# Performance work log

Hardware: AMD Instinct MI355X
Metric: run time of the kernel (lower is better)

Reference implementation:

```python
import jax, jax.numpy as jnp
import numpy as np

N, IN, C, H, NC, E, G = 4096, 16, 128, 2, 4, 131072, 64
EPS = 1e-5


def setup_inputs() -> dict:
    key = jax.random.key(0)
    ks = jax.random.split(key, 12)
    def rn(k, shape, scale=0.05):
        return jax.random.normal(k, shape, dtype=jnp.float32) * scale
    return dict(
        x=rn(ks[0], (N, IN), 1.0),
        edge_index=jax.random.randint(ks[1], (2, E), 0, N, dtype=jnp.int32),
        batch=jnp.sort(jax.random.randint(ks[2], (N,), 0, G, dtype=jnp.int32)),
        proj_W=rn(ks[3], (IN, C)), proj_b=jnp.zeros((C,), jnp.float32),
        gcn_W=rn(ks[4], (2, C, C)), gcn_b=jnp.zeros((2, C), jnp.float32),
        attn_qkv_w=rn(ks[5], (2, 3 * C, C)), attn_qkv_b=jnp.zeros((2, 3 * C), jnp.float32),
        attn_out_w=rn(ks[6], (2, C, C)), attn_out_b=jnp.zeros((2, C), jnp.float32),
        bn_gamma=jnp.ones((2, 3, C), jnp.float32), bn_beta=jnp.zeros((2, 3, C), jnp.float32),
        mlp_W1=rn(ks[7], (2, C, 2 * C)), mlp_b1=jnp.zeros((2, 2 * C), jnp.float32),
        mlp_W2=rn(ks[8], (2, 2 * C, C)), mlp_b2=jnp.zeros((2, C), jnp.float32),
        lin_W=rn(ks[9], (C, NC)), lin_b=jnp.zeros((NC,), jnp.float32),
    )


def _bn(h, g, b):
    # PyG BatchNorm (training-mode stats over the node dim, biased var)
    mu = jnp.mean(h, axis=0)
    var = jnp.mean((h - mu) ** 2, axis=0)
    return (h - mu) * jax.lax.rsqrt(var + EPS) * g + b


def _gcn(h_in, W, b, src, dst):
    # GCNConv: x' = D^-1/2 (A+I) D^-1/2 (x W) + b
    h = h_in @ W
    deg = jnp.zeros((N,), h.dtype).at[dst].add(1.0) + 1.0  # +1 self loop
    dinv = jax.lax.rsqrt(deg)
    coef = dinv[src] * dinv[dst]                           # [E]
    out = jax.ops.segment_sum(h[src] * coef[:, None], dst, num_segments=N)
    out = out + h * (dinv * dinv)[:, None]                 # self-loop term
    return out + b


def _mha(x, wqkv, bqkv, wout, bout):
    # batch=None in the source => attention over all N nodes as one sequence
    qkv = x @ wqkv.T + bqkv                                # [N,3C]
    q, k, v = jnp.split(qkv, 3, axis=-1)
    dh = C // H
    q = q.reshape(N, H, dh) * (dh ** -0.5)
    k = k.reshape(N, H, dh)
    v = v.reshape(N, H, dh)
    a = jax.nn.softmax(jnp.einsum('nhd,mhd->hnm', q, k), axis=-1)  # [H,N,N]
    o = jnp.einsum('hnm,mhd->nhd', a, v).reshape(N, C)
    return o @ wout.T + bout


def _forward(x, proj_W, proj_b, gcn_W, gcn_b, attn_qkv_w, attn_qkv_b,
             attn_out_w, attn_out_b, bn_gamma, bn_beta, mlp_W1, mlp_b1,
             mlp_W2, mlp_b2, lin_W, lin_b, edge_index, batch):
    src, dst = edge_index[0], edge_index[1]
    h = x @ proj_W + proj_b
    for l in range(2):  # two structurally-distinct GPS layers
        hl = _bn(_gcn(h, gcn_W[l], gcn_b[l], src, dst) + h, bn_gamma[l, 0], bn_beta[l, 0])
        ha = _bn(_mha(h, attn_qkv_w[l], attn_qkv_b[l], attn_out_w[l], attn_out_b[l]) + h,
                 bn_gamma[l, 1], bn_beta[l, 1])
        o = hl + ha
        m = jax.nn.relu(o @ mlp_W1[l] + mlp_b1[l]) @ mlp_W2[l] + mlp_b2[l]
        h = _bn(o + m, bn_gamma[l, 2], bn_beta[l, 2])
        if l == 0:
            h = jax.nn.relu(h)
    ssum = jax.ops.segment_sum(h, batch, num_segments=G)
    cnt = jax.ops.segment_sum(jnp.ones((N,), h.dtype), batch, num_segments=G)
    pooled = ssum / jnp.maximum(cnt, 1.0)[:, None]
    return pooled @ lin_W + lin_b


def reference(x, edge_index, batch, proj_W, proj_b, gcn_W, gcn_b,
              attn_qkv_w, attn_qkv_b, attn_out_w, attn_out_b,
              bn_gamma, bn_beta, mlp_W1, mlp_b1, mlp_W2, mlp_b2,
              lin_W, lin_b):
    return _forward(x, proj_W, proj_b, gcn_W, gcn_b, attn_qkv_w, attn_qkv_b,
                    attn_out_w, attn_out_b, bn_gamma, bn_beta, mlp_W1, mlp_b1,
                    mlp_W2, mlp_b2, lin_W, lin_b, edge_index, batch)
```

## Files before the change

kernel.cpp:

```cpp
#include <hip/hip_runtime.h>
#include <hip/hip_bf16.h>


constexpr int N_  = 4096;
constexpr int IN_ = 16;
constexpr int C_  = 128;
constexpr int E_  = 131072;
constexpr int G_  = 64;
constexpr float EPSV = 1e-5f;
constexpr int SP_ = 8;

typedef unsigned short u16;
typedef __attribute__((ext_vector_type(8))) short bf16x8;
typedef __attribute__((ext_vector_type(8))) unsigned short u16x8;
typedef __attribute__((ext_vector_type(4))) float f32x4;

__device__ inline u16 f2bf(float f) {
  union { __hip_bfloat16 b; u16 u; } v;
  v.b = __float2bfloat16(f);
  return v.u;
}
__device__ inline float bf2f(u16 s) {
  union { unsigned u; float f; } v; v.u = ((unsigned)s) << 16;
  return v.f;
}

__global__ __launch_bounds__(256) void proj_k(const float* __restrict__ x,
                                              const float* __restrict__ W,
                                              const float* __restrict__ b,
                                              float* __restrict__ h) {
  int idx = blockIdx.x * 256 + threadIdx.x;
  int n = idx >> 7, c = idx & 127;
  float acc = b[c];
#pragma unroll
  for (int k = 0; k < IN_; ++k) acc = fmaf(x[n * IN_ + k], W[k * C_ + c], acc);
  h[idx] = acc;
}

__global__ __launch_bounds__(256) void count_k(const int* __restrict__ ei,
                                               int* __restrict__ cnt) {
  int e = blockIdx.x * 256 + threadIdx.x;
  atomicAdd(&cnt[ei[E_ + e]], 1);
}
__global__ __launch_bounds__(256) void scan_k(const int* __restrict__ cnt,
                                              int* __restrict__ rowptr,
                                              int* __restrict__ cursor,
                                              float* __restrict__ dinv) {
  __shared__ int part[256];
  const int t = threadIdx.x;
  int v[16], s = 0;
#pragma unroll
  for (int i = 0; i < 16; ++i) { v[i] = cnt[t * 16 + i]; s += v[i]; }
  part[t] = s;
  __syncthreads();
  if (t == 0) {
    int run = 0;
    for (int i = 0; i < 256; ++i) { int x = part[i]; part[i] = run; run += x; }
  }
  __syncthreads();
  int off = part[t];
#pragma unroll
  for (int i = 0; i < 16; ++i) {
    int n = t * 16 + i;
    rowptr[n] = off; cursor[n] = off;
    dinv[n] = rsqrtf((float)v[i] + 1.0f);
    off += v[i];
  }
  if (t == 0) rowptr[N_] = E_;
}
__global__ __launch_bounds__(256) void fill_k(const int* __restrict__ ei,
                                              int* __restrict__ cursor,
                                              int* __restrict__ csr) {
  int e = blockIdx.x * 256 + threadIdx.x;
  int d = ei[E_ + e];
  int slot = atomicAdd(&cursor[d], 1);
  csr[slot] = ei[e];
}

__global__ __launch_bounds__(256) void wprep_k(const float* __restrict__ gcnW,
                                               const float* __restrict__ qkvW,
                                               const float* __restrict__ outW,
                                               const float* __restrict__ w1,
                                               const float* __restrict__ w2,
                                               u16* __restrict__ Wh,
                                               u16* __restrict__ Wl) {
  int bx = blockIdx.x;
  int l = bx / 144, b = bx % 144;
  const float* src; int dstOff, K, M, trans;
  if (b < 16)       { src = gcnW + l * 16384; dstOff = 0;      K = 128; M = 128; trans = 0; }
  else if (b < 64)  { src = qkvW + l * 49152; dstOff = 16384;  K = 128; M = 0;   trans = 1; b -= 16; }
  else if (b < 80)  { src = outW + l * 16384; dstOff = 65536;  K = 128; M = 0;   trans = 1; b -= 64; }
  else if (b < 112) { src = w1 + l * 32768;   dstOff = 81920;  K = 128; M = 256; trans = 0; b -= 80; }
  else              { src = w2 + l * 32768;   dstOff = 114688; K = 256; M = 128; trans = 0; b -= 112; }
  dstOff += l * 147456;
  int d = b * 1024 + threadIdx.x * 4;
  float v[4];
  if (trans) {
    const float4 f = *(const float4*)&src[d];
    v[0] = f.x; v[1] = f.y; v[2] = f.z; v[3] = f.w;
  } else {
    int ks = (K == 256) ? 8 : 7;
    int n = d >> ks, k = d & (K - 1);
#pragma unroll
    for (int j = 0; j < 4; ++j) v[j] = src[(size_t)(k + j) * M + n];
  }
  ushort4 hv, lv;
  u16* hp = (u16*)&hv; u16* lp = (u16*)&lv;
#pragma unroll
  for (int j = 0; j < 4; ++j) {
    u16 hh = f2bf(v[j]); hp[j] = hh; lp[j] = f2bf(v[j] - bf2f(hh));
  }
  *(ushort4*)&Wh[dstOff + d] = hv;
  *(ushort4*)&Wl[dstOff + d] = lv;
}

__global__ __launch_bounds__(256) void mgemm_dual_k(const float* __restrict__ A,
                                                    const u16* __restrict__ Bh,
                                                    const u16* __restrict__ Bl,
                                                    const float* __restrict__ qkvB,
                                                    float* __restrict__ t0,
                                                    u16* __restrict__ Qg,
                                                    u16* __restrict__ Kg,
                                                    u16* __restrict__ Vtg) {
  constexpr int LD = 72, K = 128;
  __shared__ u16 Ah[64 * LD], Al[64 * LD], Bsh[64 * LD], Bsl[64 * LD];
  const int tid = threadIdx.x;
  const int row0 = blockIdx.y * 64, col0 = blockIdx.x * 64;
  const int wv = tid >> 6, ln = tid & 63, quad = ln >> 4, c = ln & 15;
  f32x4 acc[4];
#pragma unroll
  for (int i = 0; i < 4; ++i) acc[i] = (f32x4){0.f, 0.f, 0.f, 0.f};

  for (int kt = 0; kt < K; kt += 64) {
    __syncthreads();
#pragma unroll
    for (int i = 0; i < 2; ++i) {
      int ch = tid + i * 256, r = ch >> 3, part = ch & 7;
      const float4 f0 = *(const float4*)&A[(size_t)(row0 + r) * K + kt + part * 8];
      const float4 f1 = *(const float4*)&A[(size_t)(row0 + r) * K + kt + part * 8 + 4];
      float fv[8] = {f0.x, f0.y, f0.z, f0.w, f1.x, f1.y, f1.z, f1.w};
      __attribute__((aligned(16))) u16 hb[8], lb[8];
#pragma unroll
      for (int j = 0; j < 8; ++j) {
        u16 hh = f2bf(fv[j]); hb[j] = hh; lb[j] = f2bf(fv[j] - bf2f(hh));
      }
      *(u16x8*)&Ah[r * LD + part * 8] = *(u16x8*)hb;
      *(u16x8*)&Al[r * LD + part * 8] = *(u16x8*)lb;
      size_t bo = (size_t)(col0 + r) * K + kt + part * 8;
      *(u16x8*)&Bsh[r * LD + part * 8] = *(const u16x8*)&Bh[bo];
      *(u16x8*)&Bsl[r * LD + part * 8] = *(const u16x8*)&Bl[bo];
    }
    __syncthreads();
#pragma unroll
    for (int kq = 0; kq < 2; ++kq) {
      bf16x8 ah = *(const bf16x8*)&Ah[(wv * 16 + c) * LD + kq * 32 + quad * 8];
      bf16x8 al = *(const bf16x8*)&Al[(wv * 16 + c) * LD + kq * 32 + quad * 8];
#pragma unroll
      for (int cb = 0; cb < 4; ++cb) {
        bf16x8 bh = *(const bf16x8*)&Bsh[(cb * 16 + c) * LD + kq * 32 + quad * 8];
        bf16x8 bl = *(const bf16x8*)&Bsl[(cb * 16 + c) * LD + kq * 32 + quad * 8];
        acc[cb] = __builtin_amdgcn_mfma_f32_16x16x32_bf16(al, bh, acc[cb], 0, 0, 0);
        acc[cb] = __builtin_amdgcn_mfma_f32_16x16x32_bf16(ah, bl, acc[cb], 0, 0, 0);
        acc[cb] = __builtin_amdgcn_mfma_f32_16x16x32_bf16(ah, bh, acc[cb], 0, 0, 0);
      }
    }
  }

  const int cls = blockIdx.x;
  if (cls < 2) {
#pragma unroll
    for (int cb = 0; cb < 4; ++cb)
#pragma unroll
      for (int r = 0; r < 4; ++r) {
        int rr = row0 + wv * 16 + quad * 4 + r;
        t0[(size_t)rr * 128 + col0 + cb * 16 + c] = acc[cb][r];
      }
  } else if (cls < 6) {
    const int isQ = cls < 4, h = cls & 1;
    const float sc = isQ ? 0.125f : 1.0f;
    u16* dst = isQ ? Qg : Kg;
#pragma unroll
    for (int cb = 0; cb < 4; ++cb) {
      int d = cb * 16 + c;
      float qb = qkvB[col0 - 128 + d];
#pragma unroll
      for (int r = 0; r < 4; ++r) {
        int rr = row0 + wv * 16 + quad * 4 + r;
        dst[((size_t)(h * N_ + rr)) * 64 + d] = f2bf((acc[cb][r] + qb) * sc);
      }
    }
  } else {
    const int h = cls & 1;
    u16* vtile = Ah;
    __syncthreads();
#pragma unroll
    for (int cb = 0; cb < 4; ++cb) {
      int d = cb * 16 + c;
      float vb = qkvB[col0 - 128 + d];
#pragma unroll
      for (int r = 0; r < 4; ++r)
        vtile[(wv * 16 + quad * 4 + r) * LD + d] = f2bf(acc[cb][r] + vb);
    }
    __syncthreads();
    int d = tid >> 2, j = tid & 3;
    __attribute__((aligned(16))) u16 buf[16];
#pragma unroll
    for (int m = 0; m < 16; ++m) buf[m] = vtile[(j * 16 + m) * LD + d];
    size_t o = ((size_t)(h * 64 + d)) * N_ + row0 + j * 16;
    *(u16x8*)&Vtg[o]     = *(u16x8*)&buf[0];
    *(u16x8*)&Vtg[o + 8] = *(u16x8*)&buf[8];
  }
}

__global__ __launch_bounds__(256) void mgemm_k(const float* __restrict__ A,
                                               const u16* __restrict__ Bh,
                                               const u16* __restrict__ Bl,
                                               const float* __restrict__ bias,
                                               float* __restrict__ Cout,
                                               int K, int Ncols, int relu,
                                               const float* __restrict__ resid,
                                               float* __restrict__ sums) {
  constexpr int LD = 72;
  __shared__ u16 Ah[64 * LD], Al[64 * LD], Bsh[64 * LD], Bsl[64 * LD];
  const int tid = threadIdx.x;
  const int row0 = blockIdx.y * 64, col0 = blockIdx.x * 64;
  const int wv = tid >> 6, ln = tid & 63, quad = ln >> 4, c = ln & 15;
  f32x4 acc[4];
#pragma unroll
  for (int i = 0; i < 4; ++i) acc[i] = (f32x4){0.f, 0.f, 0.f, 0.f};

  for (int kt = 0; kt < K; kt += 64) {
    __syncthreads();
#pragma unroll
    for (int i = 0; i < 2; ++i) {
      int ch = tid + i * 256, r = ch >> 3, part = ch & 7;
      const float4 f0 = *(const float4*)&A[(size_t)(row0 + r) * K + kt + part * 8];
      const float4 f1 = *(const float4*)&A[(size_t)(row0 + r) * K + kt + part * 8 + 4];
      float fv[8] = {f0.x, f0.y, f0.z, f0.w, f1.x, f1.y, f1.z, f1.w};
      __attribute__((aligned(16))) u16 hb[8], lb[8];
#pragma unroll
      for (int j = 0; j < 8; ++j) {
        u16 hh = f2bf(fv[j]); hb[j] = hh; lb[j] = f2bf(fv[j] - bf2f(hh));
      }
      *(u16x8*)&Ah[r * LD + part * 8] = *(u16x8*)hb;
      *(u16x8*)&Al[r * LD + part * 8] = *(u16x8*)lb;
      size_t bo = (size_t)(col0 + r) * K + kt + part * 8;
      *(u16x8*)&Bsh[r * LD + part * 8] = *(const u16x8*)&Bh[bo];
      *(u16x8*)&Bsl[r * LD + part * 8] = *(const u16x8*)&Bl[bo];
    }
    __syncthreads();
#pragma unroll
    for (int kq = 0; kq < 2; ++kq) {
      bf16x8 ah = *(const bf16x8*)&Ah[(wv * 16 + c) * LD + kq * 32 + quad * 8];
      bf16x8 al = *(const bf16x8*)&Al[(wv * 16 + c) * LD + kq * 32 + quad * 8];
#pragma unroll
      for (int cb = 0; cb < 4; ++cb) {
        bf16x8 bh = *(const bf16x8*)&Bsh[(cb * 16 + c) * LD + kq * 32 + quad * 8];
        bf16x8 bl = *(const bf16x8*)&Bsl[(cb * 16 + c) * LD + kq * 32 + quad * 8];
        acc[cb] = __builtin_amdgcn_mfma_f32_16x16x32_bf16(al, bh, acc[cb], 0, 0, 0);
        acc[cb] = __builtin_amdgcn_mfma_f32_16x16x32_bf16(ah, bl, acc[cb], 0, 0, 0);
        acc[cb] = __builtin_amdgcn_mfma_f32_16x16x32_bf16(ah, bh, acc[cb], 0, 0, 0);
      }
    }
  }
#pragma unroll
  for (int cb = 0; cb < 4; ++cb) {
    float s = 0.0f, s2 = 0.0f;
#pragma unroll
    for (int r = 0; r < 4; ++r) {
      int rr = row0 + wv * 16 + quad * 4 + r;
      int cc = col0 + cb * 16 + c;
      float o = acc[cb][r] + (bias ? bias[cc] : 0.0f);
      if (resid) o += resid[(size_t)rr * Ncols + cc];
      if (relu) o = fmaxf(o, 0.0f);
      Cout[(size_t)rr * Ncols + cc] = o;
      s += o; s2 = fmaf(o, o, s2);
    }
    if (sums) {
      s  += __shfl_xor(s, 16);  s  += __shfl_xor(s, 32);
      s2 += __shfl_xor(s2, 16); s2 += __shfl_xor(s2, 32);
      if (quad == 0) {
        int cc = col0 + cb * 16 + c;
        atomicAdd(&sums[cc], s);
        atomicAdd(&sums[C_ + cc], s2);
      }
    }
  }
}

__global__ __launch_bounds__(256) void mgemm_attn_k(const float* __restrict__ attnP,
                                                    const float* __restrict__ accLp,
                                                    const u16* __restrict__ Bh,
                                                    const u16* __restrict__ Bl,
                                                    const float* __restrict__ bias,
                                                    float* __restrict__ Cout,
                                                    const float* __restrict__ resid,
                                                    float* __restrict__ sums) {
  constexpr int LD = 72, K = 128;
  __shared__ u16 Ah[64 * LD], Al[64 * LD], Bsh[64 * LD], Bsl[64 * LD];
  const int tid = threadIdx.x;
  const int row0 = blockIdx.y * 64, col0 = blockIdx.x * 64;
  const int wv = tid >> 6, ln = tid & 63, quad = ln >> 4, c = ln & 15;
  f32x4 acc[4];
#pragma unroll
  for (int i = 0; i < 4; ++i) acc[i] = (f32x4){0.f, 0.f, 0.f, 0.f};

  for (int kt = 0; kt < K; kt += 64) {
    const int head = kt >> 6;
    __syncthreads();
#pragma unroll
    for (int i = 0; i < 2; ++i) {
      int ch = tid + i * 256, r = ch >> 3, part = ch & 7;
      float lsum = 0.0f;
#pragma unroll
      for (int sp = 0; sp < SP_; ++sp) lsum += accLp[(sp * 2 + head) * N_ + row0 + r];
      float invl = 1.0f / lsum;
      float fv[8] = {0.f, 0.f, 0.f, 0.f, 0.f, 0.f, 0.f, 0.f};
#pragma unroll
      for (int sp = 0; sp < SP_; ++sp) {
        const float* p = &attnP[((size_t)sp * N_ + row0 + r) * C_ + kt + part * 8];
        const float4 f0 = *(const float4*)p;
        const float4 f1 = *(const float4*)(p + 4);
        fv[0] += f0.x; fv[1] += f0.y; fv[2] += f0.z; fv[3] += f0.w;
        fv[4] += f1.x; fv[5] += f1.y; fv[6] += f1.z; fv[7] += f1.w;
      }
      __attribute__((aligned(16))) u16 hb[8], lb[8];
#pragma unroll
      for (int j = 0; j < 8; ++j) {
        float f = fv[j] * invl;
        u16 hh = f2bf(f); hb[j] = hh; lb[j] = f2bf(f - bf2f(hh));
      }
      *(u16x8*)&Ah[r * LD + part * 8] = *(u16x8*)hb;
      *(u16x8*)&Al[r * LD + part * 8] = *(u16x8*)lb;
      size_t bo = (size_t)(col0 + r) * K + kt + part * 8;
      *(u16x8*)&Bsh[r * LD + part * 8] = *(const u16x8*)&Bh[bo];
      *(u16x8*)&Bsl[r * LD + part * 8] = *(const u16x8*)&Bl[bo];
    }
    __syncthreads();
#pragma unroll
    for (int kq = 0; kq < 2; ++kq) {
      bf16x8 ah = *(const bf16x8*)&Ah[(wv * 16 + c) * LD + kq * 32 + quad * 8];
      bf16x8 al = *(const bf16x8*)&Al[(wv * 16 + c) * LD + kq * 32 + quad * 8];
#pragma unroll
      for (int cb = 0; cb < 4; ++cb) {
        bf16x8 bh = *(const bf16x8*)&Bsh[(cb * 16 + c) * LD + kq * 32 + quad * 8];
        bf16x8 bl = *(const bf16x8*)&Bsl[(cb * 16 + c) * LD + kq * 32 + quad * 8];
        acc[cb] = __builtin_amdgcn_mfma_f32_16x16x32_bf16(al, bh, acc[cb], 0, 0, 0);
        acc[cb] = __builtin_amdgcn_mfma_f32_16x16x32_bf16(ah, bl, acc[cb], 0, 0, 0);
        acc[cb] = __builtin_amdgcn_mfma_f32_16x16x32_bf16(ah, bh, acc[cb], 0, 0, 0);
      }
    }
  }
#pragma unroll
  for (int cb = 0; cb < 4; ++cb) {
    float s = 0.0f, s2 = 0.0f;
#pragma unroll
    for (int r = 0; r < 4; ++r) {
      int rr = row0 + wv * 16 + quad * 4 + r;
      int cc = col0 + cb * 16 + c;
      float o = acc[cb][r] + bias[cc] + resid[(size_t)rr * 128 + cc];
      Cout[(size_t)rr * 128 + cc] = o;
      s += o; s2 = fmaf(o, o, s2);
    }
    s  += __shfl_xor(s, 16);  s  += __shfl_xor(s, 32);
    s2 += __shfl_xor(s2, 16); s2 += __shfl_xor(s2, 32);
    if (quad == 0) {
      int cc = col0 + cb * 16 + c;
      atomicAdd(&sums[cc], s);
      atomicAdd(&sums[C_ + cc], s2);
    }
  }
}

__global__ __launch_bounds__(128) void gcn_gather_k(const int* __restrict__ rowptr,
                                                    const int* __restrict__ csr,
                                                    const float* __restrict__ hw,
                                                    const float* __restrict__ dinv,
                                                    const float* __restrict__ b,
                                                    const float* __restrict__ hres,
                                                    float* __restrict__ out) {
  const int n = blockIdx.x, c = threadIdx.x;
  const float din = dinv[n];
  float acc = fmaf(hw[(size_t)n * C_ + c], din * din, b[c] + hres[(size_t)n * C_ + c]);
  const int e1 = rowptr[n + 1];
  for (int e = rowptr[n]; e < e1; ++e) {
    int s = csr[e];
    acc = fmaf(hw[(size_t)s * C_ + c], dinv[s] * din, acc);
  }
  out[(size_t)n * C_ + c] = acc;
}

__global__ __launch_bounds__(256) void bn_stats_k(const float* __restrict__ A,
                                                  float* __restrict__ sums) {
  int c = threadIdx.x & 127, half = threadIdx.x >> 7;
  int r0 = blockIdx.x * 16 + half * 8;
  float s = 0.0f, s2 = 0.0f;
#pragma unroll
  for (int i = 0; i < 8; ++i) {
    float v = A[(size_t)(r0 + i) * C_ + c];
    s += v;
    s2 = fmaf(v, v, s2);
  }
  __shared__ float ls[256], ls2[256];
  ls[threadIdx.x] = s; ls2[threadIdx.x] = s2;
  __syncthreads();
  if (half == 0) {
    atomicAdd(&sums[c], s + ls[c + 128]);
    atomicAdd(&sums[C_ + c], s2 + ls2[c + 128]);
  }
}

__global__ __launch_bounds__(256) void bn_finapply2_k(const float* __restrict__ t0,
                                                      const float* __restrict__ t1,
                                                      const float* __restrict__ sums1,
                                                      const float* __restrict__ sums0,
                                                      const float* __restrict__ g1,
                                                      const float* __restrict__ b1v,
                                                      const float* __restrict__ g0,
                                                      const float* __restrict__ b0v,
                                                      float* __restrict__ ob) {
  __shared__ float scl1[128], shf1[128], scl0[128], shf0[128];
  const int t = threadIdx.x;
  if (t < 128) {
    float mu = sums1[t] * (1.0f / N_);
    float var = sums1[C_ + t] * (1.0f / N_) - mu * mu;
    float sc = rsqrtf(var + EPSV) * g1[t];
    scl1[t] = sc; shf1[t] = fmaf(-mu, sc, b1v[t]);
    mu = sums0[t] * (1.0f / N_);
    var = sums0[C_ + t] * (1.0f / N_) - mu * mu;
    sc = rsqrtf(var + EPSV) * g0[t];
    scl0[t] = sc; shf0[t] = fmaf(-mu, sc, b0v[t]);
  }
  __syncthreads();
  int idx = blockIdx.x * 256 + t;
  int c = idx & 127;
  ob[idx] = fmaf(t0[idx], scl1[c], shf1[c]) + fmaf(t1[idx], scl0[c], shf0[c]);
}

__global__ __launch_bounds__(256) void bn_finapply_k(const float* __restrict__ A,
                                                     const float* __restrict__ sums,
                                                     const float* __restrict__ g,
                                                     const float* __restrict__ b,
                                                     float* __restrict__ outp, int relu,
                                                     const int* __restrict__ batch,
                                                     float* __restrict__ pooled) {
  __shared__ float s_scl[128], s_shf[128];
  const int t = threadIdx.x;
  if (t < 128) {
    float mu = sums[t] * (1.0f / N_);
    float var = sums[C_ + t] * (1.0f / N_) - mu * mu;
    float sc = rsqrtf(var + EPSV) * g[t];
    s_scl[t] = sc;
    s_shf[t] = fmaf(-mu, sc, b[t]);
  }
  __syncthreads();
  int idx = blockIdx.x * 256 + t;
  int c = idx & 127;
  float v = fmaf(A[idx], s_scl[c], s_shf[c]);
  if (relu) v = fmaxf(v, 0.0f);
  outp[idx] = v;
  if (pooled) {
    int n = idx >> 7;
    atomicAdd(&pooled[(size_t)batch[n] * C_ + c], v);
  }
}

__global__ __launch_bounds__(256) void flash_mfma_k(const u16* __restrict__ Qg,
                                                    const u16* __restrict__ Kg,
                                                    const u16* __restrict__ Vtg,
                                                    float* __restrict__ attnP,
                                                    float* __restrict__ accLp) {
  constexpr int LD = 72;
  __shared__ u16 Ks[64 * LD], Vts[64 * LD], Ps[64 * LD];
  const int tid = threadIdx.x;
  const int h = blockIdx.z, sp = blockIdx.y, q0 = blockIdx.x * 64;
  const int wv = tid >> 6, ln = tid & 63, quad = ln >> 4, c = ln & 15;
  const int KPS = N_ / SP_;

  bf16x8 qf[2];
#pragma unroll
  for (int kq = 0; kq < 2; ++kq)
    qf[kq] = *(const bf16x8*)&Qg[((size_t)(h * N_ + q0 + wv * 16 + c)) * 64 + kq * 32 + quad * 8];

  f32x4 O[4];
#pragma unroll
  for (int i = 0; i < 4; ++i) O[i] = (f32x4){0.f, 0.f, 0.f, 0.f};
  float l4[4] = {0.f, 0.f, 0.f, 0.f};
  u16* Pw = &Ps[wv * 16 * LD];

  for (int it = 0; it < KPS / 64; ++it) {
    const int k0 = sp * KPS + it * 64;
    __syncthreads();
#pragma unroll
    for (int i = 0; i < 2; ++i) {
      int ch = tid + i * 256, row = ch >> 3, part = ch & 7;
      *(u16x8*)&Ks[row * LD + part * 8] =
          *(const u16x8*)&Kg[((size_t)(h * N_ + k0 + row)) * 64 + part * 8];
      *(u16x8*)&Vts[row * LD + part * 8] =
          *(const u16x8*)&Vtg[((size_t)(h * 64 + row)) * N_ + k0 + part * 8];
    }
    __syncthreads();

#pragma unroll
    for (int kb = 0; kb < 4; ++kb) {
      f32x4 s = (f32x4){0.f, 0.f, 0.f, 0.f};
#pragma unroll
      for (int kq = 0; kq < 2; ++kq) {
        bf16x8 b = *(const bf16x8*)&Ks[(kb * 16 + c) * LD + kq * 32 + quad * 8];
        s = __builtin_amdgcn_mfma_f32_16x16x32_bf16(qf[kq], b, s, 0, 0, 0);
      }
#pragma unroll
      for (int r = 0; r < 4; ++r) {
        u16 ph = f2bf(__expf(s[r] - 8.0f));
        l4[r] += bf2f(ph);
        Pw[(quad * 4 + r) * LD + kb * 16 + c] = ph;
      }
    }
#pragma unroll
    for (int db = 0; db < 4; ++db) {
#pragma unroll
      for (int kq = 0; kq < 2; ++kq) {
        bf16x8 a = *(const bf16x8*)&Pw[c * LD + kq * 32 + quad * 8];
        bf16x8 b = *(const bf16x8*)&Vts[(db * 16 + c) * LD + kq * 32 + quad * 8];
        O[db] = __builtin_amdgcn_mfma_f32_16x16x32_bf16(a, b, O[db], 0, 0, 0);
      }
    }
  }

#pragma unroll
  for (int r = 0; r < 4; ++r) {
#pragma unroll
    for (int off = 1; off < 16; off <<= 1) l4[r] += __shfl_xor(l4[r], off);
  }

#pragma unroll
  for (int db = 0; db < 4; ++db)
#pragma unroll
    for (int r = 0; r < 4; ++r) {
      int q = q0 + wv * 16 + quad * 4 + r;
      attnP[((size_t)sp * N_ + q) * C_ + h * 64 + db * 16 + c] = O[db][r];
    }
  if (c == 0) {
#pragma unroll
    for (int r = 0; r < 4; ++r)
      accLp[(sp * 2 + h) * N_ + q0 + wv * 16 + quad * 4 + r] = l4[r];
  }
}

__global__ __launch_bounds__(256) void final_k(const float* __restrict__ pooled,
                                               const int* __restrict__ batch,
                                               const float* __restrict__ W,
                                               const float* __restrict__ b,
                                               float* __restrict__ out) {
  int t = threadIdx.x;
  int g = t >> 2, j = t & 3;
  int lo = 0, hi = N_;
  while (lo < hi) { int m = (lo + hi) >> 1; if (batch[m] < g) lo = m + 1; else hi = m; }
  int st = lo; lo = 0; hi = N_;
  while (lo < hi) { int m = (lo + hi) >> 1; if (batch[m] < g + 1) lo = m + 1; else hi = m; }
  float inv = 1.0f / fmaxf((float)(lo - st), 1.0f);
  float acc = b[j];
  for (int c = 0; c < C_; ++c) acc = fmaf(pooled[(size_t)g * C_ + c] * inv, W[c * 4 + j], acc);
  out[t] = acc;
}

extern "C" void kernel_launch(void* const* d_in, const int* in_sizes, int n_in,
                              void* d_out, int out_size, void* d_ws, size_t ws_size,
                              hipStream_t stream) {
  const float* x     = (const float*)d_in[0];
  const int*   ei    = (const int*)d_in[1];
  const int*   batch = (const int*)d_in[2];
  const float* projW = (const float*)d_in[3];
  const float* projB = (const float*)d_in[4];
  const float* gcnW  = (const float*)d_in[5];
  const float* gcnB  = (const float*)d_in[6];
  const float* qkvW  = (const float*)d_in[7];
  const float* qkvB  = (const float*)d_in[8];
  const float* outW  = (const float*)d_in[9];
  const float* outB  = (const float*)d_in[10];
  const float* bnG   = (const float*)d_in[11];
  const float* bnB   = (const float*)d_in[12];
  const float* w1    = (const float*)d_in[13];
  const float* b1    = (const float*)d_in[14];
  const float* w2    = (const float*)d_in[15];
  const float* b2    = (const float*)d_in[16];
  const float* linW  = (const float*)d_in[17];
  const float* linB  = (const float*)d_in[18];
  float* out = (float*)d_out;

  const size_t NC = (size_t)N_ * C_;
  const size_t HB = (size_t)2 * N_ * 64;
  float* ws   = (float*)d_ws;
  float* h    = ws;
  float* t0   = ws + 1 * NC;
  float* t1   = ws + 2 * NC;
  float* ob   = ws + 3 * NC;
  u16* Qg  = (u16*)(ws + 4 * NC);
  u16* Kg  = Qg + HB;
  u16* Vtg = Kg + HB;
  float* attnP = ws + 6 * NC;
  float* m1b   = attnP;
  float* accLp = ws + (6 + SP_) * NC;
  float* sums  = accLp + 2 * SP_ * N_;
  float* pooled = sums + 6 * 256;
  int*   icnt = (int*)(pooled + (size_t)G_ * C_);
  float* dinv = (float*)(icnt + N_);
  int*   rowptr = (int*)(dinv + N_);
  int*   cursor = rowptr + N_ + 1;
  int*   csr    = cursor + N_;
  u16*   Wh = (u16*)(csr + E_);
  u16*   Wl = Wh + 2 * 147456;

  const dim3 b256(256);

  hipMemsetAsync(sums, 0, (6 * 256 + (size_t)G_ * C_ + N_) * sizeof(float), stream);

  count_k<<<E_ / 256, b256, 0, stream>>>(ei, icnt);
  scan_k<<<1, b256, 0, stream>>>(icnt, rowptr, cursor, dinv);
  fill_k<<<E_ / 256, b256, 0, stream>>>(ei, cursor, csr);

  proj_k<<<(int)(NC / 256), b256, 0, stream>>>(x, projW, projB, h);
  wprep_k<<<288, b256, 0, stream>>>(gcnW, qkvW, outW, w1, w2, Wh, Wl);

  for (int l = 0; l < 2; ++l) {
    const size_t WL = (size_t)l * 147456;
    float* sums0 = sums + (l * 3 + 0) * 256;
    float* sums1 = sums + (l * 3 + 1) * 256;
    float* sums2 = sums + (l * 3 + 2) * 256;

    mgemm_dual_k<<<dim3(8, 64), b256, 0, stream>>>(h, Wh + WL, Wl + WL,
                                                   qkvB + l * 384, t0, Qg, Kg, Vtg);
    gcn_gather_k<<<N_, dim3(128), 0, stream>>>(rowptr, csr, t0, dinv, gcnB + l * C_, h, t1);
    bn_stats_k<<<N_ / 16, b256, 0, stream>>>(t1, sums0);
    flash_mfma_k<<<dim3(N_ / 64, SP_, 2), b256, 0, stream>>>(Qg, Kg, Vtg, attnP, accLp);
    mgemm_attn_k<<<dim3(2, 64), b256, 0, stream>>>(attnP, accLp,
                                                   Wh + WL + 65536, Wl + WL + 65536,
                                                   outB + l * C_, t0, h, sums1);
    bn_finapply2_k<<<(int)(NC / 256), b256, 0, stream>>>(
        t0, t1, sums1, sums0,
        bnG + (l * 3 + 1) * C_, bnB + (l * 3 + 1) * C_,
        bnG + (l * 3 + 0) * C_, bnB + (l * 3 + 0) * C_, ob);
    mgemm_k<<<dim3(4, 64), b256, 0, stream>>>(ob, Wh + WL + 81920, Wl + WL + 81920,
                                              b1 + l * 256, m1b, 128, 256, 1,
                                              nullptr, nullptr);
    mgemm_k<<<dim3(2, 64), b256, 0, stream>>>(m1b, Wh + WL + 114688, Wl + WL + 114688,
                                              b2 + l * C_, t0, 256, 128, 0,
                                              ob, sums2);
    bn_finapply_k<<<(int)(NC / 256), b256, 0, stream>>>(
        t0, sums2, bnG + (l * 3 + 2) * C_, bnB + (l * 3 + 2) * C_, h,
        (l == 0) ? 1 : 0, batch, (l == 1) ? pooled : nullptr);
  }

  final_k<<<1, 256, 0, stream>>>(pooled, batch, linW, linB, out);
}
```

Before: 340.0 us.

## Merge prologue, CSR fill and GCN/attention branches into fewer heterogeneous launches

Proj, weight prep and degree counting now run in one prologue launch. The CSR fill is folded into the layer-0 QKV GEMM launch as extra blocks. The GCN gather with BN stats and the flash attention share one launch with interleaved block roles. This removes several kernel launches and their serialization gaps, and lets the memory-bound gather overlap the MFMA-bound attention. In exchange, blocks of different kinds share one shared-memory and register budget, and the BN stats reduction is now done per 4-node block.

```diff
diff --git a/kernel.cpp b/kernel.cpp
--- a/kernel.cpp
+++ b/kernel.cpp
@@ -25,23 +25,65 @@
   return v.f;
 }
 
-__global__ __launch_bounds__(256) void proj_k(const float* __restrict__ x,
-                                              const float* __restrict__ W,
-                                              const float* __restrict__ b,
-                                              float* __restrict__ h) {
-  int idx = blockIdx.x * 256 + threadIdx.x;
-  int n = idx >> 7, c = idx & 127;
-  float acc = b[c];
-#pragma unroll
-  for (int k = 0; k < IN_; ++k) acc = fmaf(x[n * IN_ + k], W[k * C_ + c], acc);
-  h[idx] = acc;
-}
-
-__global__ __launch_bounds__(256) void count_k(const int* __restrict__ ei,
-                                               int* __restrict__ cnt) {
-  int e = blockIdx.x * 256 + threadIdx.x;
-  atomicAdd(&cnt[ei[E_ + e]], 1);
-}
+__global__ __launch_bounds__(256) void prol_k(const float* __restrict__ x,
+                                              const float* __restrict__ projW,
+                                              const float* __restrict__ projB,
+                                              float* __restrict__ h,
+                                              const float* __restrict__ gcnW,
+                                              const float* __restrict__ qkvW,
+                                              const float* __restrict__ outW,
+                                              const float* __restrict__ w1,
+                                              const float* __restrict__ w2,
+                                              u16* __restrict__ Wh,
+                                              u16* __restrict__ Wl,
+                                              const int* __restrict__ ei,
+                                              int* __restrict__ cnt) {
+  const int bx = blockIdx.x;
+  const int tid = threadIdx.x;
+  if (bx < 2048) {
+    int idx = bx * 256 + tid;
+    int n = idx >> 7, c = idx & 127;
+    float acc = projB[c];
+#pragma unroll
+    for (int k = 0; k < IN_; ++k) acc = fmaf(x[n * IN_ + k], projW[k * C_ + c], acc);
+    h[idx] = acc;
+    return;
+  }
+  if (bx >= 2336) {
+    int e = (bx - 2336) * 256 + tid;
+    atomicAdd(&cnt[ei[E_ + e]], 1);
+    return;
+  }
+  int wb = bx - 2048;
+  int l = wb / 144, b = wb % 144;
+  const float* src; int dstOff, K, M, trans;
+  if (b < 16)       { src = gcnW + l * 16384; dstOff = 0;      K = 128; M = 128; trans = 0; }
+  else if (b < 64)  { src = qkvW + l * 49152; dstOff = 16384;  K = 128; M = 0;   trans = 1; b -= 16; }
+  else if (b < 80)  { src = outW + l * 16384; dstOff = 65536;  K = 128; M = 0;   trans = 1; b -= 64; }
+  else if (b < 112) { src = w1 + l * 32768;   dstOff = 81920;  K = 128; M = 256; trans = 0; b -= 80; }
+  else              { src = w2 + l * 32768;   dstOff = 114688; K = 256; M = 128; trans = 0; b -= 112; }
+  dstOff += l * 147456;
+  int d = b * 1024 + tid * 4;
+  float v[4];
+  if (trans) {
+    const float4 f = *(const float4*)&src[d];
+    v[0] = f.x; v[1] = f.y; v[2] = f.z; v[3] = f.w;
+  } else {
+    int ks = (K == 256) ? 8 : 7;
+    int n = d >> ks, k = d & (K - 1);
+#pragma unroll
+    for (int j = 0; j < 4; ++j) v[j] = src[(size_t)(k + j) * M + n];
+  }
+  ushort4 hv, lv;
+  u16* hp = (u16*)&hv; u16* lp = (u16*)&lv;
+#pragma unroll
+  for (int j = 0; j < 4; ++j) {
+    u16 hh = f2bf(v[j]); hp[j] = hh; lp[j] = f2bf(v[j] - bf2f(hh));
+  }
+  *(ushort4*)&Wh[dstOff + d] = hv;
+  *(ushort4*)&Wl[dstOff + d] = lv;
+}
+
 __global__ __launch_bounds__(256) void scan_k(const int* __restrict__ cnt,
                                               int* __restrict__ rowptr,
                                               int* __restrict__ cursor,
@@ -68,51 +110,6 @@
   }
   if (t == 0) rowptr[N_] = E_;
 }
-__global__ __launch_bounds__(256) void fill_k(const int* __restrict__ ei,
-                                              int* __restrict__ cursor,
-                                              int* __restrict__ csr) {
-  int e = blockIdx.x * 256 + threadIdx.x;
-  int d = ei[E_ + e];
-  int slot = atomicAdd(&cursor[d], 1);
-  csr[slot] = ei[e];
-}
-
-__global__ __launch_bounds__(256) void wprep_k(const float* __restrict__ gcnW,
-                                               const float* __restrict__ qkvW,
-                                               const float* __restrict__ outW,
-                                               const float* __restrict__ w1,
-                                               const float* __restrict__ w2,
-                                               u16* __restrict__ Wh,
-                                               u16* __restrict__ Wl) {
-  int bx = blockIdx.x;
-  int l = bx / 144, b = bx % 144;
-  const float* src; int dstOff, K, M, trans;
-  if (b < 16)       { src = gcnW + l * 16384; dstOff = 0;      K = 128; M = 128; trans = 0; }
-  else if (b < 64)  { src = qkvW + l * 49152; dstOff = 16384;  K = 128; M = 0;   trans = 1; b -= 16; }
-  else if (b < 80)  { src = outW + l * 16384; dstOff = 65536;  K = 128; M = 0;   trans = 1; b -= 64; }
-  else if (b < 112) { src = w1 + l * 32768;   dstOff = 81920;  K = 128; M = 256; trans = 0; b -= 80; }
-  else              { src = w2 + l * 32768;   dstOff = 114688; K = 256; M = 128; trans = 0; b -= 112; }
-  dstOff += l * 147456;
-  int d = b * 1024 + threadIdx.x * 4;
-  float v[4];
-  if (trans) {
-    const float4 f = *(const float4*)&src[d];
-    v[0] = f.x; v[1] = f.y; v[2] = f.z; v[3] = f.w;
-  } else {
-    int ks = (K == 256) ? 8 : 7;
-    int n = d >> ks, k = d & (K - 1);
-#pragma unroll
-    for (int j = 0; j < 4; ++j) v[j] = src[(size_t)(k + j) * M + n];
-  }
-  ushort4 hv, lv;
-  u16* hp = (u16*)&hv; u16* lp = (u16*)&lv;
-#pragma unroll
-  for (int j = 0; j < 4; ++j) {
-    u16 hh = f2bf(v[j]); hp[j] = hh; lp[j] = f2bf(v[j] - bf2f(hh));
-  }
-  *(ushort4*)&Wh[dstOff + d] = hv;
-  *(ushort4*)&Wl[dstOff + d] = lv;
-}
 
 __global__ __launch_bounds__(256) void mgemm_dual_k(const float* __restrict__ A,
                                                     const u16* __restrict__ Bh,
@@ -121,11 +118,22 @@
                                                     float* __restrict__ t0,
                                                     u16* __restrict__ Qg,
                                                     u16* __restrict__ Kg,
-                                                    u16* __restrict__ Vtg) {
+                                                    u16* __restrict__ Vtg,
+                                                    const int* __restrict__ ei,
+                                                    int* __restrict__ cursor,
+                                                    int* __restrict__ csr) {
   constexpr int LD = 72, K = 128;
   __shared__ u16 Ah[64 * LD], Al[64 * LD], Bsh[64 * LD], Bsl[64 * LD];
+  const int bx = blockIdx.x;
   const int tid = threadIdx.x;
-  const int row0 = blockIdx.y * 64, col0 = blockIdx.x * 64;
+  if (bx >= 512) {
+    int e = (bx - 512) * 256 + tid;
+    int d = ei[E_ + e];
+    int slot = atomicAdd(&cursor[d], 1);
+    csr[slot] = ei[e];
+    return;
+  }
+  const int row0 = (bx >> 3) * 64, col0 = (bx & 7) * 64;
   const int wv = tid >> 6, ln = tid & 63, quad = ln >> 4, c = ln & 15;
   f32x4 acc[4];
 #pragma unroll
@@ -166,7 +174,7 @@
     }
   }
 
-  const int cls = blockIdx.x;
+  const int cls = bx & 7;
   if (cls < 2) {
 #pragma unroll
     for (int cb = 0; cb < 4; ++cb)
@@ -176,7 +184,7 @@
         t0[(size_t)rr * 128 + col0 + cb * 16 + c] = acc[cb][r];
       }
   } else if (cls < 6) {
-    const int isQ = cls < 4, h = cls & 1;
+    const int isQ = cls < 4, hd = cls & 1;
     const float sc = isQ ? 0.125f : 1.0f;
     u16* dst = isQ ? Qg : Kg;
 #pragma unroll
@@ -186,11 +194,11 @@
 #pragma unroll
       for (int r = 0; r < 4; ++r) {
         int rr = row0 + wv * 16 + quad * 4 + r;
-        dst[((size_t)(h * N_ + rr)) * 64 + d] = f2bf((acc[cb][r] + qb) * sc);
+        dst[((size_t)(hd * N_ + rr)) * 64 + d] = f2bf((acc[cb][r] + qb) * sc);
       }
     }
   } else {
-    const int h = cls & 1;
+    const int hd = cls & 1;
     u16* vtile = Ah;
     __syncthreads();
 #pragma unroll
@@ -206,7 +214,7 @@
     __attribute__((aligned(16))) u16 buf[16];
 #pragma unroll
     for (int m = 0; m < 16; ++m) buf[m] = vtile[(j * 16 + m) * LD + d];
-    size_t o = ((size_t)(h * 64 + d)) * N_ + row0 + j * 16;
+    size_t o = ((size_t)(hd * 64 + d)) * N_ + row0 + j * 16;
     *(u16x8*)&Vtg[o]     = *(u16x8*)&buf[0];
     *(u16x8*)&Vtg[o + 8] = *(u16x8*)&buf[8];
   }
@@ -372,41 +380,132 @@
   }
 }
 
-__global__ __launch_bounds__(128) void gcn_gather_k(const int* __restrict__ rowptr,
-                                                    const int* __restrict__ csr,
-                                                    const float* __restrict__ hw,
-                                                    const float* __restrict__ dinv,
-                                                    const float* __restrict__ b,
-                                                    const float* __restrict__ hres,
-                                                    float* __restrict__ out) {
-  const int n = blockIdx.x, c = threadIdx.x;
-  const float din = dinv[n];
-  float acc = fmaf(hw[(size_t)n * C_ + c], din * din, b[c] + hres[(size_t)n * C_ + c]);
-  const int e1 = rowptr[n + 1];
-  for (int e = rowptr[n]; e < e1; ++e) {
-    int s = csr[e];
-    acc = fmaf(hw[(size_t)s * C_ + c], dinv[s] * din, acc);
-  }
-  out[(size_t)n * C_ + c] = acc;
-}
-
-__global__ __launch_bounds__(256) void bn_stats_k(const float* __restrict__ A,
-                                                  float* __restrict__ sums) {
-  int c = threadIdx.x & 127, half = threadIdx.x >> 7;
-  int r0 = blockIdx.x * 16 + half * 8;
-  float s = 0.0f, s2 = 0.0f;
-#pragma unroll
-  for (int i = 0; i < 8; ++i) {
-    float v = A[(size_t)(r0 + i) * C_ + c];
-    s += v;
-    s2 = fmaf(v, v, s2);
-  }
-  __shared__ float ls[256], ls2[256];
-  ls[threadIdx.x] = s; ls2[threadIdx.x] = s2;
-  __syncthreads();
-  if (half == 0) {
-    atomicAdd(&sums[c], s + ls[c + 128]);
-    atomicAdd(&sums[C_ + c], s2 + ls2[c + 128]);
+__global__ __launch_bounds__(256) void branch_k(const u16* __restrict__ Qg,
+                                                const u16* __restrict__ Kg,
+                                                const u16* __restrict__ Vtg,
+                                                float* __restrict__ attnP,
+                                                float* __restrict__ accLp,
+                                                const int* __restrict__ rowptr,
+                                                const int* __restrict__ csr,
+                                                const float* __restrict__ hw,
+                                                const float* __restrict__ dinv,
+                                                const float* __restrict__ gbias,
+                                                const float* __restrict__ hres,
+                                                float* __restrict__ t1,
+                                                float* __restrict__ sums0) {
+  constexpr int LD = 72;
+  __shared__ __attribute__((aligned(16))) u16 smem[3 * 64 * LD];
+  const int tid = threadIdx.x;
+  const int bx = blockIdx.x;
+
+  if (bx & 1) {
+    const int b = bx >> 1;
+    const int wq = tid >> 6, lane = tid & 63;
+    const int n = b * 4 + wq;
+    float* ls  = (float*)smem;
+    float* ls2 = ls + 512;
+    const float din = dinv[n];
+    float a0 = fmaf(hw[(size_t)n * C_ + lane], din * din,
+                    gbias[lane] + hres[(size_t)n * C_ + lane]);
+    float a1 = fmaf(hw[(size_t)n * C_ + lane + 64], din * din,
+                    gbias[lane + 64] + hres[(size_t)n * C_ + lane + 64]);
+    const int e1 = rowptr[n + 1];
+    for (int e = rowptr[n]; e < e1; ++e) {
+      int si = csr[e];
+      float w = dinv[si] * din;
+      a0 = fmaf(hw[(size_t)si * C_ + lane], w, a0);
+      a1 = fmaf(hw[(size_t)si * C_ + lane + 64], w, a1);
+    }
+    t1[(size_t)n * C_ + lane]      = a0;
+    t1[(size_t)n * C_ + lane + 64] = a1;
+    ls[wq * 128 + lane]       = a0;  ls[wq * 128 + lane + 64]  = a1;
+    ls2[wq * 128 + lane]      = a0 * a0;
+    ls2[wq * 128 + lane + 64] = a1 * a1;
+    __syncthreads();
+    if (tid < 128) {
+      float s  = ls[tid]  + ls[tid + 128]  + ls[tid + 256]  + ls[tid + 384];
+      float s2 = ls2[tid] + ls2[tid + 128] + ls2[tid + 256] + ls2[tid + 384];
+      atomicAdd(&sums0[tid], s);
+      atomicAdd(&sums0[C_ + tid], s2);
+    }
+    return;
+  }
+
+  u16* Ks  = smem;
+  u16* Vts = smem + 64 * LD;
+  u16* Ps  = smem + 2 * 64 * LD;
+  const int fb = bx >> 1;
+  const int head = fb >> 9, sp = (fb >> 6) & 7, q0 = (fb & 63) * 64;
+  const int wv = tid >> 6, ln = tid & 63, quad = ln >> 4, c = ln & 15;
+  const int KPS = N_ / SP_;
+
+  bf16x8 qf[2];
+#pragma unroll
+  for (int kq = 0; kq < 2; ++kq)
+    qf[kq] = *(const bf16x8*)&Qg[((size_t)(head * N_ + q0 + wv * 16 + c)) * 64 + kq * 32 + quad * 8];
+
+  f32x4 O[4];
+#pragma unroll
+  for (int i = 0; i < 4; ++i) O[i] = (f32x4){0.f, 0.f, 0.f, 0.f};
+  float l4[4] = {0.f, 0.f, 0.f, 0.f};
+  u16* Pw = &Ps[wv * 16 * LD];
+
+  for (int it = 0; it < KPS / 64; ++it) {
+    const int k0 = sp * KPS + it * 64;
+    __syncthreads();
+#pragma unroll
+    for (int i = 0; i < 2; ++i) {
+      int ch = tid + i * 256, row = ch >> 3, part = ch & 7;
+      *(u16x8*)&Ks[row * LD + part * 8] =
+          *(const u16x8*)&Kg[((size_t)(head * N_ + k0 + row)) * 64 + part * 8];
+      *(u16x8*)&Vts[row * LD + part * 8] =
+          *(const u16x8*)&Vtg[((size_t)(head * 64 + row)) * N_ + k0 + part * 8];
+    }
+    __syncthreads();
+
+#pragma unroll
+    for (int kb = 0; kb < 4; ++kb) {
+      f32x4 s = (f32x4){0.f, 0.f, 0.f, 0.f};
+#pragma unroll
+      for (int kq = 0; kq < 2; ++kq) {
+        bf16x8 b = *(const bf16x8*)&Ks[(kb * 16 + c) * LD + kq * 32 + quad * 8];
+        s = __builtin_amdgcn_mfma_f32_16x16x32_bf16(qf[kq], b, s, 0, 0, 0);
+      }
+#pragma unroll
+      for (int r = 0; r < 4; ++r) {
+        u16 ph = f2bf(__expf(s[r] - 8.0f));
+        l4[r] += bf2f(ph);
+        Pw[(quad * 4 + r) * LD + kb * 16 + c] = ph;
+      }
+    }
+#pragma unroll
+    for (int db = 0; db < 4; ++db) {
+#pragma unroll
+      for (int kq = 0; kq < 2; ++kq) {
+        bf16x8 a = *(const bf16x8*)&Pw[c * LD + kq * 32 + quad * 8];
+        bf16x8 b = *(const bf16x8*)&Vts[(db * 16 + c) * LD + kq * 32 + quad * 8];
+        O[db] = __builtin_amdgcn_mfma_f32_16x16x32_bf16(a, b, O[db], 0, 0, 0);
+      }
+    }
+  }
+
+#pragma unroll
+  for (int r = 0; r < 4; ++r) {
+#pragma unroll
+    for (int off = 1; off < 16; off <<= 1) l4[r] += __shfl_xor(l4[r], off);
+  }
+
+#pragma unroll
+  for (int db = 0; db < 4; ++db)
+#pragma unroll
+    for (int r = 0; r < 4; ++r) {
+      int q = q0 + wv * 16 + quad * 4 + r;
+      attnP[((size_t)sp * N_ + q) * C_ + head * 64 + db * 16 + c] = O[db][r];
+    }
+  if (c == 0) {
+#pragma unroll
+    for (int r = 0; r < 4; ++r)
+      accLp[(sp * 2 + head) * N_ + q0 + wv * 16 + quad * 4 + r] = l4[r];
   }
 }
 
@@ -462,88 +561,6 @@
   if (pooled) {
     int n = idx >> 7;
     atomicAdd(&pooled[(size_t)batch[n] * C_ + c], v);
-  }
-}
-
-__global__ __launch_bounds__(256) void flash_mfma_k(const u16* __restrict__ Qg,
-                                                    const u16* __restrict__ Kg,
-                                                    const u16* __restrict__ Vtg,
-                                                    float* __restrict__ attnP,
-                                                    float* __restrict__ accLp) {
-  constexpr int LD = 72;
-  __shared__ u16 Ks[64 * LD], Vts[64 * LD], Ps[64 * LD];
-  const int tid = threadIdx.x;
-  const int h = blockIdx.z, sp = blockIdx.y, q0 = blockIdx.x * 64;
-  const int wv = tid >> 6, ln = tid & 63, quad = ln >> 4, c = ln & 15;
-  const int KPS = N_ / SP_;
-
-  bf16x8 qf[2];
-#pragma unroll
-  for (int kq = 0; kq < 2; ++kq)
-    qf[kq] = *(const bf16x8*)&Qg[((size_t)(h * N_ + q0 + wv * 16 + c)) * 64 + kq * 32 + quad * 8];
-
-  f32x4 O[4];
-#pragma unroll
-  for (int i = 0; i < 4; ++i) O[i] = (f32x4){0.f, 0.f, 0.f, 0.f};
-  float l4[4] = {0.f, 0.f, 0.f, 0.f};
-  u16* Pw = &Ps[wv * 16 * LD];
-
-  for (int it = 0; it < KPS / 64; ++it) {
-    const int k0 = sp * KPS + it * 64;
-    __syncthreads();
-#pragma unroll
-    for (int i = 0; i < 2; ++i) {
-      int ch = tid + i * 256, row = ch >> 3, part = ch & 7;
-      *(u16x8*)&Ks[row * LD + part * 8] =
-          *(const u16x8*)&Kg[((size_t)(h * N_ + k0 + row)) * 64 + part * 8];
-      *(u16x8*)&Vts[row * LD + part * 8] =
-          *(const u16x8*)&Vtg[((size_t)(h * 64 + row)) * N_ + k0 + part * 8];
-    }
-    __syncthreads();
-
-#pragma unroll
-    for (int kb = 0; kb < 4; ++kb) {
-      f32x4 s = (f32x4){0.f, 0.f, 0.f, 0.f};
-#pragma unroll
-      for (int kq = 0; kq < 2; ++kq) {
-        bf16x8 b = *(const bf16x8*)&Ks[(kb * 16 + c) * LD + kq * 32 + quad * 8];
-        s = __builtin_amdgcn_mfma_f32_16x16x32_bf16(qf[kq], b, s, 0, 0, 0);
-      }
-#pragma unroll
-      for (int r = 0; r < 4; ++r) {
-        u16 ph = f2bf(__expf(s[r] - 8.0f));
-        l4[r] += bf2f(ph);
-        Pw[(quad * 4 + r) * LD + kb * 16 + c] = ph;
-      }
-    }
-#pragma unroll
-    for (int db = 0; db < 4; ++db) {
-#pragma unroll
-      for (int kq = 0; kq < 2; ++kq) {
-        bf16x8 a = *(const bf16x8*)&Pw[c * LD + kq * 32 + quad * 8];
-        bf16x8 b = *(const bf16x8*)&Vts[(db * 16 + c) * LD + kq * 32 + quad * 8];
-        O[db] = __builtin_amdgcn_mfma_f32_16x16x32_bf16(a, b, O[db], 0, 0, 0);
-      }
-    }
-  }
-
-#pragma unroll
-  for (int r = 0; r < 4; ++r) {
-#pragma unroll
-    for (int off = 1; off < 16; off <<= 1) l4[r] += __shfl_xor(l4[r], off);
-  }
-
-#pragma unroll
-  for (int db = 0; db < 4; ++db)
-#pragma unroll
-    for (int r = 0; r < 4; ++r) {
-      int q = q0 + wv * 16 + quad * 4 + r;
-      attnP[((size_t)sp * N_ + q) * C_ + h * 64 + db * 16 + c] = O[db][r];
-    }
-  if (c == 0) {
-#pragma unroll
-    for (int r = 0; r < 4; ++r)
-      accLp[(sp * 2 + h) * N_ + q0 + wv * 16 + quad * 4 + r] = l4[r];
   }
 }
 
@@ -615,12 +632,9 @@
 
   hipMemsetAsync(sums, 0, (6 * 256 + (size_t)G_ * C_ + N_) * sizeof(float), stream);
 
-  count_k<<<E_ / 256, b256, 0, stream>>>(ei, icnt);
+  prol_k<<<2848, b256, 0, stream>>>(x, projW, projB, h, gcnW, qkvW, outW,
+                                    w1, w2, Wh, Wl, ei, icnt);
   scan_k<<<1, b256, 0, stream>>>(icnt, rowptr, cursor, dinv);
-  fill_k<<<E_ / 256, b256, 0, stream>>>(ei, cursor, csr);
-
-  proj_k<<<(int)(NC / 256), b256, 0, stream>>>(x, projW, projB, h);
-  wprep_k<<<288, b256, 0, stream>>>(gcnW, qkvW, outW, w1, w2, Wh, Wl);
 
   for (int l = 0; l < 2; ++l) {
     const size_t WL = (size_t)l * 147456;
@@ -628,11 +642,11 @@
     float* sums1 = sums + (l * 3 + 1) * 256;
     float* sums2 = sums + (l * 3 + 2) * 256;
 
-    mgemm_dual_k<<<dim3(8, 64), b256, 0, stream>>>(h, Wh + WL, Wl + WL,
-                                                   qkvB + l * 384, t0, Qg, Kg, Vtg);
-    gcn_gather_k<<<N_, dim3(128), 0, stream>>>(rowptr, csr, t0, dinv, gcnB + l * C_, h, t1);
-    bn_stats_k<<<N_ / 16, b256, 0, stream>>>(t1, sums0);
-    flash_mfma_k<<<dim3(N_ / 64, SP_, 2), b256, 0, stream>>>(Qg, Kg, Vtg, attnP, accLp);
+    mgemm_dual_k<<<(l == 0) ? 1024 : 512, b256, 0, stream>>>(
+        h, Wh + WL, Wl + WL, qkvB + l * 384, t0, Qg, Kg, Vtg, ei, cursor, csr);
+    branch_k<<<2048, b256, 0, stream>>>(Qg, Kg, Vtg, attnP, accLp,
+                                        rowptr, csr, t0, dinv, gcnB + l * C_,
+                                        h, t1, sums0);
     mgemm_attn_k<<<dim3(2, 64), b256, 0, stream>>>(attnP, accLp,
                                                    Wh + WL + 65536, Wl + WL + 65536,
                                                    outB + l * C_, t0, h, sums1);
```

New measurement: 318.4 us. 1.07x faster.
